# Kernel tuning notes

Measured on AMD Instinct MI355X. Metric: run time of the kernel, lower is better.

## Reference

```python
import jax, jax.numpy as jnp
import numpy as np

D_MODEL = 1024
D_STATE = 16
D_CONV = 4
D_INNER = 2 * D_MODEL          # expand * d_model
DT_RANK = (D_MODEL + 15) // 16 # ceil(d_model/16) = 64
BATCH, SEQLEN = 2, 1024


def setup_inputs() -> dict:
    key = jax.random.key(0)
    ks = jax.random.split(key, 8)
    s = lambda k, shape, scale=0.02: (jax.random.normal(k, shape, jnp.float32) * scale)
    return {
        "hidden_states": jax.random.normal(ks[0], (BATCH, SEQLEN, D_MODEL), jnp.float32),
        "in_proj_w": s(ks[1], (2 * D_INNER, D_MODEL)),
        "conv_w": s(ks[2], (D_INNER, 1, D_CONV), 0.3),   # depthwise conv kernel (O, I/groups=1, K)
        "conv_b": jnp.zeros((D_INNER,), jnp.float32),
        "x_proj_w": s(ks[3], (DT_RANK + 2 * D_STATE, D_INNER)),
        "dt_proj_w": s(ks[4], (D_INNER, DT_RANK), 0.1),
        # inverse-softplus of small dt values, like the torch init
        "dt_proj_b": jax.random.uniform(ks[5], (D_INNER,), jnp.float32, minval=-5.0, maxval=-2.0),
        "A_log": jnp.log(jnp.broadcast_to(jnp.arange(1, D_STATE + 1, dtype=jnp.float32), (D_INNER, D_STATE))),
        "D": jnp.ones((D_INNER,), jnp.float32),
        "out_proj_w": s(ks[6], (D_MODEL, D_INNER)),
    }


def _forward(hidden_states, in_proj_w, conv_w, conv_b, x_proj_w,
             dt_proj_w, dt_proj_b, A_log, D, out_proj_w):
    B, L, _ = hidden_states.shape
    # in_proj -> split into x, z
    xz = hidden_states @ in_proj_w.T                      # [B, L, 2*d_inner]
    x, z = jnp.split(xz, 2, axis=-1)
    # causal depthwise conv1d (pad left d_conv-1, then take first L) + SiLU
    xc = jnp.transpose(x, (0, 2, 1))                      # [B, d_inner, L]
    xc = jax.lax.conv_general_dilated(
        xc, conv_w, window_strides=(1,), padding=[(D_CONV - 1, 0)],
        feature_group_count=D_INNER,
        dimension_numbers=("NCH", "OIH", "NCH")) + conv_b[None, :, None]
    xc = jax.nn.silu(xc)
    u = jnp.transpose(xc, (0, 2, 1)).astype(jnp.float32)  # [B, L, d_inner]
    # x_proj -> dt_low, B, C
    x_dbl = u @ x_proj_w.T                                # [B, L, dt_rank + 2*d_state]
    dt_low, Bp, Cp = jnp.split(x_dbl, [DT_RANK, DT_RANK + D_STATE], axis=-1)
    dt = dt_low @ dt_proj_w.T + dt_proj_b                 # [B, L, d_inner]
    # NOTE: original adds dt_proj.bias AGAIN as delta_bias inside the scan, then softplus
    delta = jax.nn.softplus(dt + dt_proj_b)
    A = -jnp.exp(A_log.astype(jnp.float32))               # [d_inner, d_state]
    # discretization
    dA = jnp.exp(jnp.einsum("bld,dn->lbdn", delta, A))    # [L, B, d, n]
    dBu = jnp.einsum("bld,bln,bld->lbdn", delta, Bp.astype(jnp.float32), u)
    C_t = jnp.transpose(Cp.astype(jnp.float32), (1, 0, 2))  # [L, B, n]

    def step(state, inp):
        a, b, c = inp
        state = a * state + b                             # [B, d, n]
        y = jnp.einsum("bdn,bn->bd", state, c)
        return state, y

    x0 = jnp.zeros((B, D_INNER, D_STATE), jnp.float32)
    _, ys = jax.lax.scan(step, x0, (dA, dBu, C_t))        # ys: [L, B, d]
    y = jnp.transpose(ys, (1, 0, 2))                      # [B, L, d]
    y = y + u * D.astype(jnp.float32)                     # skip connection
    y = y * jax.nn.silu(z.astype(jnp.float32))            # gating
    y = y.astype(hidden_states.dtype)
    return y @ out_proj_w.T                               # [B, L, d_model]


def reference(hidden_states, in_proj_w, conv_w, conv_b, x_proj_w,
              dt_proj_w, dt_proj_b, A_log, D, out_proj_w):
    return _forward(hidden_states, in_proj_w, conv_w, conv_b, x_proj_w,
                    dt_proj_w, dt_proj_b, A_log, D, out_proj_w)
```

## Files before the change

### kernel.cpp

```cpp
#include <hip/hip_runtime.h>
#include <hip/hip_bf16.h>
#include <math.h>

#define BATCH   2
#define SEQLEN  1024
#define DMODEL  1024
#define DINNER  2048
#define DSTATE  16
#define DTRANK  64
#define XPAD    128
#define MROWS   (BATCH*SEQLEN)
#define NSEG    8
#define SEGLEN  (SEQLEN/NSEG)
#define XP_SPLIT  16

typedef float    f32x4  __attribute__((ext_vector_type(4)));
typedef _Float16 f16x8  __attribute__((ext_vector_type(8)));
typedef _Float16 f16x4  __attribute__((ext_vector_type(4)));

template<int EPI>
__global__ __launch_bounds__(256) void pgemm(
    const _Float16* __restrict__ A, int lda,
    const _Float16* __restrict__ W, int ldw,
    float* __restrict__ C, int ldc, int K,
    const float* __restrict__ bias, _Float16* __restrict__ C16, size_t zstride)
{
  constexpr int APS = 520;
  constexpr int BPS = 1032;
  __shared__ _Float16 As[2][8 * APS];
  __shared__ _Float16 Bs[2][8 * BPS];

  const int t  = threadIdx.x;
  const int m0 = blockIdx.y * 64, n0 = blockIdx.x * 128;
  const int kchunk = K / gridDim.z;
  const int kbeg = blockIdx.z * kchunk;
  const int nIter = kchunk / 64;

  const int kb = t & 7;
  const int r0 = t >> 3;
  const _Float16* gA = A + (size_t)(m0 + r0) * lda + kbeg + kb * 8;
  const _Float16* gB = W + (size_t)(n0 + r0) * ldw + kbeg + kb * 8;
  const size_t a32 = (size_t)32 * lda;
  const size_t b32 = (size_t)32 * ldw;
  const int aoff = kb * APS + r0 * 8;
  const int boff = kb * BPS + r0 * 8;

  {
    f16x8 a0 = *(const f16x8*)(gA);
    f16x8 a1 = *(const f16x8*)(gA + a32);
    f16x8 b0 = *(const f16x8*)(gB);
    f16x8 b1 = *(const f16x8*)(gB + b32);
    f16x8 b2 = *(const f16x8*)(gB + 2 * b32);
    f16x8 b3 = *(const f16x8*)(gB + 3 * b32);
    gA += 64; gB += 64;
    *(f16x8*)&As[0][aoff]       = a0;
    *(f16x8*)&As[0][aoff + 256] = a1;
    *(f16x8*)&Bs[0][boff]       = b0;
    *(f16x8*)&Bs[0][boff + 256] = b1;
    *(f16x8*)&Bs[0][boff + 512] = b2;
    *(f16x8*)&Bs[0][boff + 768] = b3;
  }

  const int lane = t & 63, wvi = t >> 6;
  const int wn = wvi * 32;
  const int lm = lane & 15, lk = lane >> 4;

  f32x4 acc[4][2] = {};

  for (int it = 0; it < nIter; ++it) {
    __syncthreads();
    const bool more = (it + 1 < nIter);
    f16x8 a0, a1, b0, b1, b2, b3;
    if (more) {
      a0 = *(const f16x8*)(gA);
      a1 = *(const f16x8*)(gA + a32);
      b0 = *(const f16x8*)(gB);
      b1 = *(const f16x8*)(gB + b32);
      b2 = *(const f16x8*)(gB + 2 * b32);
      b3 = *(const f16x8*)(gB + 3 * b32);
      gA += 64; gB += 64;
    }
    const int cb = it & 1;
#pragma unroll
    for (int s = 0; s < 2; ++s) {
      f16x8 av[4], bv[2];
#pragma unroll
      for (int i = 0; i < 4; ++i)
        av[i] = *(const f16x8*)&As[cb][(s * 4 + lk) * APS + (i * 16 + lm) * 8];
#pragma unroll
      for (int j = 0; j < 2; ++j)
        bv[j] = *(const f16x8*)&Bs[cb][(s * 4 + lk) * BPS + (wn + j * 16 + lm) * 8];
#pragma unroll
      for (int i = 0; i < 4; ++i)
#pragma unroll
        for (int j = 0; j < 2; ++j)
          acc[i][j] = __builtin_amdgcn_mfma_f32_16x16x32_f16(av[i], bv[j], acc[i][j], 0, 0, 0);
    }
    if (more) {
      const int nb = (it + 1) & 1;
      *(f16x8*)&As[nb][aoff]       = a0;
      *(f16x8*)&As[nb][aoff + 256] = a1;
      *(f16x8*)&Bs[nb][boff]       = b0;
      *(f16x8*)&Bs[nb][boff + 256] = b1;
      *(f16x8*)&Bs[nb][boff + 512] = b2;
      *(f16x8*)&Bs[nb][boff + 768] = b3;
    }
  }

  float* Cz = C + (size_t)blockIdx.z * zstride;
#pragma unroll
  for (int i = 0; i < 4; ++i) {
    const int mrow = m0 + i * 16 + lk * 4;
#pragma unroll
    for (int j = 0; j < 2; ++j) {
      const int col = n0 + wn + j * 16 + lm;
#pragma unroll
      for (int r = 0; r < 4; ++r) {
        float v = acc[i][j][r];
        size_t off = (size_t)(mrow + r) * ldc + col;
        if constexpr (EPI == 0) {
          Cz[off] = v;
        } else if constexpr (EPI == 2) {
          float x = v + 2.f * bias[col];
          Cz[off] = (x > 20.f) ? x : log1pf(__expf(x));
        } else {
          C16[off] = (_Float16)v;
        }
      }
    }
  }
}

#define R0 (MROWS * DMODEL / 4)
#define R1 (2 * DINNER * DMODEL / 4)
#define R2 (DMODEL * DINNER / 4)
#define R3 (DINNER * DTRANK / 4)
#define R4 (XPAD * DINNER / 4)
#define F2H_TOTAL (R0 + R1 + R2 + R3 + R4)

__global__ __launch_bounds__(256) void f2h_all(
    const float* __restrict__ hid, const float* __restrict__ w_in,
    const float* __restrict__ w_out, const float* __restrict__ w_dt,
    const float* __restrict__ w_xp,
    _Float16* __restrict__ hid16, _Float16* __restrict__ w_in16,
    _Float16* __restrict__ w_out16, _Float16* __restrict__ w_dt16,
    _Float16* __restrict__ w_xp16)
{
  int i = blockIdx.x * 256 + threadIdx.x;
  const float* src; _Float16* dst; int off;
  if (i < R0)                     { src = hid;   dst = hid16;   off = i; }
  else if (i < R0+R1)             { src = w_in;  dst = w_in16;  off = i - R0; }
  else if (i < R0+R1+R2)          { src = w_out; dst = w_out16; off = i - (R0+R1); }
  else if (i < R0+R1+R2+R3)       { src = w_dt;  dst = w_dt16;  off = i - (R0+R1+R2); }
  else if (i < F2H_TOTAL) {
    off = i - (R0+R1+R2+R3);
    int r = (off * 4) >> 11;
    f16x4 h = {0, 0, 0, 0};
    if (r < 96) {
      float4 v = ((const float4*)w_xp)[off];
      h = (f16x4){(_Float16)v.x, (_Float16)v.y, (_Float16)v.z, (_Float16)v.w};
    }
    ((f16x4*)w_xp16)[off] = h;
    return;
  } else return;
  float4 v = ((const float4*)src)[off];
  ((f16x4*)dst)[off] = (f16x4){(_Float16)v.x, (_Float16)v.y, (_Float16)v.z, (_Float16)v.w};
}

__global__ __launch_bounds__(256) void reduce_xdbl(
    const float* __restrict__ part,
    float* __restrict__ xdbl32, _Float16* __restrict__ xdbl16)
{
  int i = blockIdx.x * 256 + threadIdx.x;
  f32x4 s = ((const f32x4*)part)[i];
#pragma unroll
  for (int z = 1; z < XP_SPLIT; ++z)
    s += ((const f32x4*)part)[(size_t)z * (MROWS * XPAD / 4) + i];
  ((f32x4*)xdbl32)[i] = s;
  int col4 = (i & 31) * 4;
  if (col4 < DTRANK) {
    int row = i >> 5;
    *(f16x4*)&xdbl16[(size_t)row * DTRANK + col4] =
        (f16x4){(_Float16)s.x, (_Float16)s.y, (_Float16)s.z, (_Float16)s.w};
  }
}

__global__ __launch_bounds__(256) void conv_silu(
    const _Float16* __restrict__ xz16,
    const float* __restrict__ conv_w,
    const float* __restrict__ conv_b,
    _Float16* __restrict__ u16)
{
  const int idx = blockIdx.x * 256 + threadIdx.x;
  const int d   = idx & (DINNER - 1);
  const int row = idx >> 11;
  const int l   = row & (SEQLEN - 1);
  float s = conv_b[d];
#pragma unroll
  for (int k = 0; k < 4; ++k) {
    int lt = l + k - 3;
    if (lt >= 0)
      s = fmaf((float)xz16[(size_t)(row + k - 3) * (2 * DINNER) + d],
               conv_w[d * 4 + k], s);
  }
  float v = s / (1.f + __expf(-s));
  u16[idx] = (_Float16)v;
}

__device__ __forceinline__ float row_sum16(float x) {
  int v = __builtin_bit_cast(int, x);
  x += __builtin_bit_cast(float, __builtin_amdgcn_update_dpp(0, v, 0x128, 0xF, 0xF, true));
  v = __builtin_bit_cast(int, x);
  x += __builtin_bit_cast(float, __builtin_amdgcn_update_dpp(0, v, 0x124, 0xF, 0xF, true));
  v = __builtin_bit_cast(int, x);
  x += __builtin_bit_cast(float, __builtin_amdgcn_update_dpp(0, v, 0x4E, 0xF, 0xF, true));
  v = __builtin_bit_cast(int, x);
  x += __builtin_bit_cast(float, __builtin_amdgcn_update_dpp(0, v, 0xB1, 0xF, 0xF, true));
  return x;
}

__global__ __launch_bounds__(256) void scan_part1(
    const float* __restrict__ delta,
    const _Float16* __restrict__ u16,
    const float* __restrict__ x_dbl,
    const float* __restrict__ A_log,
    float* __restrict__ pbuf, float* __restrict__ ebuf)
{
  const int t = threadIdx.x;
  const int c = t >> 4, n = t & 15;
  const int bb = blockIdx.x;
  const int seg = bb >> 8;
  const int r = bb & 255;
  const int b = r >> 7;
  const int d_base = (r & 127) * 16;

  const float A_dn = -__expf(A_log[(d_base + c) * DSTATE + n]);
  float s = 0.f, p = 1.f;

  __shared__ __align__(16) float dl[16 * 68];
  __shared__ __align__(16) float ul[16 * 68];
  __shared__ __align__(16) float Bl[16 * 68];

  const int i_st = t >> 2;
  const int cc = (t & 3) * 4;

  for (int l0 = seg * SEGLEN; l0 < seg * SEGLEN + SEGLEN; l0 += 64) {
    const int row = b * SEQLEN + l0 + i_st;
    {
      float4 dv = *(const float4*)&delta[(size_t)row * DINNER + d_base + cc];
      f16x4  uh = *(const f16x4*)&u16[(size_t)row * DINNER + d_base + cc];
      float4 Bv = *(const float4*)&x_dbl[(size_t)row * XPAD + DTRANK + cc];
      dl[(cc+0)*68 + i_st] = dv.x; dl[(cc+1)*68 + i_st] = dv.y;
      dl[(cc+2)*68 + i_st] = dv.z; dl[(cc+3)*68 + i_st] = dv.w;
      ul[(cc+0)*68 + i_st] = (float)uh[0]; ul[(cc+1)*68 + i_st] = (float)uh[1];
      ul[(cc+2)*68 + i_st] = (float)uh[2]; ul[(cc+3)*68 + i_st] = (float)uh[3];
      Bl[(cc+0)*68 + i_st] = Bv.x; Bl[(cc+1)*68 + i_st] = Bv.y;
      Bl[(cc+2)*68 + i_st] = Bv.z; Bl[(cc+3)*68 + i_st] = Bv.w;
    }
    __syncthreads();
#pragma unroll
    for (int i0 = 0; i0 < 64; i0 += 4) {
      f32x4 dv4 = *(const f32x4*)&dl[c * 68 + i0];
      f32x4 uv4 = *(const f32x4*)&ul[c * 68 + i0];
      f32x4 Bv4 = *(const f32x4*)&Bl[n * 68 + i0];
#pragma unroll
      for (int rr = 0; rr < 4; ++rr) {
        float dA = __expf(dv4[rr] * A_dn);
        s = fmaf(dA, s, dv4[rr] * Bv4[rr] * uv4[rr]);
        p *= dA;
      }
    }
    __syncthreads();
  }
  const int peIdx = (r * NSEG + seg) * 256 + t;
  pbuf[peIdx] = p;
  ebuf[peIdx] = s;
}

__global__ __launch_bounds__(256) void scan_part2(
    const float* __restrict__ delta,
    const _Float16* __restrict__ u16,
    const _Float16* __restrict__ xz16,
    const float* __restrict__ x_dbl,
    const float* __restrict__ A_log,
    const float* __restrict__ Dp,
    const float* __restrict__ pbuf,
    const float* __restrict__ ebuf,
    _Float16* __restrict__ y16)
{
  const int t = threadIdx.x;
  const int c = t >> 4, n = t & 15;
  const int bb = blockIdx.x;
  const int seg = bb >> 8;
  const int r = bb & 255;
  const int b = r >> 7;
  const int d_base = (r & 127) * 16;

  const float A_dn = -__expf(A_log[(d_base + c) * DSTATE + n]);

  float s = 0.f;
  {
    const int base = r * NSEG * 256 + t;
    for (int k = 0; k < seg; ++k)
      s = fmaf(pbuf[base + k * 256], s, ebuf[base + k * 256]);
  }

  __shared__ __align__(16) float dl[16 * 68];
  __shared__ __align__(16) float ul[16 * 68];
  __shared__ __align__(16) float Bl[16 * 68];
  __shared__ __align__(16) float Cl[16 * 68];
  __shared__ __align__(16) float yl[16 * 68];
  __shared__ __align__(16) float z_s[64 * 16];
  __shared__ float Dp_s[16];

  if (t < 16) Dp_s[t] = Dp[d_base + t];

  const int i_st = t >> 2;
  const int cc = (t & 3) * 4;

  for (int l0 = seg * SEGLEN; l0 < seg * SEGLEN + SEGLEN; l0 += 64) {
    const int row = b * SEQLEN + l0 + i_st;
    {
      float4 dv = *(const float4*)&delta[(size_t)row * DINNER + d_base + cc];
      f16x4  uh = *(const f16x4*)&u16[(size_t)row * DINNER + d_base + cc];
      float4 Bv = *(const float4*)&x_dbl[(size_t)row * XPAD + DTRANK + cc];
      float4 Cv = *(const float4*)&x_dbl[(size_t)row * XPAD + DTRANK + DSTATE + cc];
      f16x4  zh = *(const f16x4*)&xz16[(size_t)row * (2 * DINNER) + DINNER + d_base + cc];
      dl[(cc+0)*68 + i_st] = dv.x; dl[(cc+1)*68 + i_st] = dv.y;
      dl[(cc+2)*68 + i_st] = dv.z; dl[(cc+3)*68 + i_st] = dv.w;
      ul[(cc+0)*68 + i_st] = (float)uh[0]; ul[(cc+1)*68 + i_st] = (float)uh[1];
      ul[(cc+2)*68 + i_st] = (float)uh[2]; ul[(cc+3)*68 + i_st] = (float)uh[3];
      Bl[(cc+0)*68 + i_st] = Bv.x; Bl[(cc+1)*68 + i_st] = Bv.y;
      Bl[(cc+2)*68 + i_st] = Bv.z; Bl[(cc+3)*68 + i_st] = Bv.w;
      Cl[(cc+0)*68 + i_st] = Cv.x; Cl[(cc+1)*68 + i_st] = Cv.y;
      Cl[(cc+2)*68 + i_st] = Cv.z; Cl[(cc+3)*68 + i_st] = Cv.w;
      float4 zv = make_float4((float)zh[0], (float)zh[1], (float)zh[2], (float)zh[3]);
      *(float4*)&z_s[t * 4] = zv;
    }
    __syncthreads();

#pragma unroll
    for (int i0 = 0; i0 < 64; i0 += 4) {
      f32x4 dv4 = *(const f32x4*)&dl[c * 68 + i0];
      f32x4 uv4 = *(const f32x4*)&ul[c * 68 + i0];
      f32x4 Bv4 = *(const f32x4*)&Bl[n * 68 + i0];
      f32x4 Cv4 = *(const f32x4*)&Cl[n * 68 + i0];
      f32x4 py;
#pragma unroll
      for (int rr = 0; rr < 4; ++rr) {
        float dA = __expf(dv4[rr] * A_dn);
        s = fmaf(dA, s, dv4[rr] * Bv4[rr] * uv4[rr]);
        py[rr] = row_sum16(s * Cv4[rr]);
      }
      if (n == 0) *(f32x4*)&yl[c * 68 + i0] = py;
    }
    __syncthreads();

#pragma unroll
    for (int k = 0; k < 4; ++k) {
      int o = t + 256 * k;
      int i = o >> 4, c2 = o & 15;
      float ssum = yl[c2 * 68 + i];
      float uv = ul[c2 * 68 + i];
      float zv = z_s[o];
      float yv = fmaf(uv, Dp_s[c2], ssum);
      yv *= zv / (1.f + __expf(-zv));
      y16[(size_t)(b * SEQLEN + l0 + i) * DINNER + d_base + c2] = (_Float16)yv;
    }
    __syncthreads();
  }
}

extern "C" void kernel_launch(void* const* d_in, const int* in_sizes, int n_in,
                              void* d_out, int out_size, void* d_ws, size_t ws_size,
                              hipStream_t stream)
{
  const float* hidden     = (const float*)d_in[0];
  const float* in_proj_w  = (const float*)d_in[1];
  const float* conv_w     = (const float*)d_in[2];
  const float* conv_b     = (const float*)d_in[3];
  const float* x_proj_w   = (const float*)d_in[4];
  const float* dt_proj_w  = (const float*)d_in[5];
  const float* dt_proj_b  = (const float*)d_in[6];
  const float* A_log      = (const float*)d_in[7];
  const float* Dp         = (const float*)d_in[8];
  const float* out_proj_w = (const float*)d_in[9];
  float* out = (float*)d_out;

  char* p = (char*)d_ws;
  _Float16* xz16   = (_Float16*)p;  p += (size_t)MROWS * 2 * DINNER * 2;
  _Float16* u16    = (_Float16*)p;  p += (size_t)MROWS * DINNER * 2;
  float*    xdbl32 = (float*)p;     p += (size_t)MROWS * XPAD * 4;
  float*    delta  = (float*)p;     p += (size_t)MROWS * DINNER * 4;
  _Float16* h16    = (_Float16*)p;  p += (size_t)MROWS * DMODEL * 2;
  _Float16* win16  = (_Float16*)p;  p += (size_t)2 * DINNER * DMODEL * 2;
  _Float16* wout16 = (_Float16*)p;  p += (size_t)DMODEL * DINNER * 2;
  _Float16* wdt16  = (_Float16*)p;  p += (size_t)DINNER * DTRANK * 2;
  _Float16* wxp16  = (_Float16*)p;  p += (size_t)XPAD * DINNER * 2;
  _Float16* xdbl16 = (_Float16*)p;  p += (size_t)MROWS * DTRANK * 2;
  _Float16* y16    = (_Float16*)p;  p += (size_t)MROWS * DINNER * 2;
  float*    pbuf   = (float*)p;     p += (size_t)256 * NSEG * 256 * 4;
  float*    ebuf   = (float*)p;     p += (size_t)256 * NSEG * 256 * 4;
  float*    xp_part = delta;

  f2h_all<<<(F2H_TOTAL + 255) / 256, 256, 0, stream>>>(
      hidden, in_proj_w, out_proj_w, dt_proj_w, x_proj_w,
      h16, win16, wout16, wdt16, wxp16);

  pgemm<4><<<dim3(2 * DINNER / 128, MROWS / 64, 1), 256, 0, stream>>>(
      h16, DMODEL, win16, DMODEL, nullptr, 2 * DINNER, DMODEL, nullptr, xz16, 0);

  conv_silu<<<(MROWS * DINNER) / 256, 256, 0, stream>>>(xz16, conv_w, conv_b, u16);

  pgemm<0><<<dim3(1, MROWS / 64, XP_SPLIT), 256, 0, stream>>>(
      u16, DINNER, wxp16, DINNER, xp_part, XPAD, DINNER, nullptr, nullptr,
      (size_t)MROWS * XPAD);

  reduce_xdbl<<<(MROWS * XPAD / 4) / 256, 256, 0, stream>>>(xp_part, xdbl32, xdbl16);

  pgemm<2><<<dim3(DINNER / 128, MROWS / 64, 1), 256, 0, stream>>>(
      xdbl16, DTRANK, wdt16, DTRANK, delta, DINNER, DTRANK, dt_proj_b, nullptr, 0);

  scan_part1<<<256 * NSEG, 256, 0, stream>>>(delta, u16, xdbl32, A_log, pbuf, ebuf);
  scan_part2<<<256 * NSEG, 256, 0, stream>>>(delta, u16, xz16, xdbl32, A_log, Dp,
                                             pbuf, ebuf, y16);

  pgemm<0><<<dim3(DMODEL / 128, MROWS / 64, 1), 256, 0, stream>>>(
      y16, DINNER, wout16, DINNER, out, DMODEL, DINNER, nullptr, nullptr, 0);
}
```

Before: 252.6 us.

## Add 128x128-tile GEMM for in_proj and split-K out_proj with reduction

Adds a 128x128 block-tile MFMA GEMM kernel with four 64x64 warp tiles and uses it for the large in_proj GEMM, so each operand load from global memory feeds more MFMAs. The out_proj GEMM also moves to the larger tile, but with a 2-way K split writing partials into the now-dead xz16 buffer, followed by a separate reduce kernel. The larger tiles cut the grid size, which the out_proj split-K is meant to offset. The cost is an extra launch plus extra fp32 traffic for the partial sums, and higher register and LDS use per block, which lowers occupancy.

Result: no change. 250.7 us (-0.7%).

```diff
diff --git a/kernel.cpp b/kernel.cpp
--- a/kernel.cpp
+++ b/kernel.cpp
@@ -13,13 +13,14 @@
 #define NSEG    8
 #define SEGLEN  (SEQLEN/NSEG)
 #define XP_SPLIT  16
+#define OUT_SPLIT 2
 
 typedef float    f32x4  __attribute__((ext_vector_type(4)));
 typedef _Float16 f16x8  __attribute__((ext_vector_type(8)));
 typedef _Float16 f16x4  __attribute__((ext_vector_type(4)));
 
 template<int EPI>
-__global__ __launch_bounds__(256) void pgemm(
+__global__ __launch_bounds__(256) void pgemm64(
     const _Float16* __restrict__ A, int lda,
     const _Float16* __restrict__ W, int ldw,
     float* __restrict__ C, int ldc, int K,
@@ -120,9 +121,112 @@
         size_t off = (size_t)(mrow + r) * ldc + col;
         if constexpr (EPI == 0) {
           Cz[off] = v;
-        } else if constexpr (EPI == 2) {
+        } else {
           float x = v + 2.f * bias[col];
           Cz[off] = (x > 20.f) ? x : log1pf(__expf(x));
+        }
+      }
+    }
+  }
+}
+
+template<int EPI>
+__global__ __launch_bounds__(256) void pgemm128(
+    const _Float16* __restrict__ A, int lda,
+    const _Float16* __restrict__ W, int ldw,
+    float* __restrict__ C, int ldc, int K,
+    _Float16* __restrict__ C16, size_t zstride)
+{
+  constexpr int PS = 1032;
+  __shared__ _Float16 As[2][8 * PS];
+  __shared__ _Float16 Bs[2][8 * PS];
+
+  const int t  = threadIdx.x;
+  const int m0 = blockIdx.y * 128, n0 = blockIdx.x * 128;
+  const int kchunk = K / gridDim.z;
+  const int kbeg = blockIdx.z * kchunk;
+  const int nIter = kchunk / 64;
+
+  const int kb = t & 7;
+  const int r0 = t >> 3;
+  const _Float16* gA = A + (size_t)(m0 + r0) * lda + kbeg + kb * 8;
+  const _Float16* gB = W + (size_t)(n0 + r0) * ldw + kbeg + kb * 8;
+  const size_t a32 = (size_t)32 * lda;
+  const size_t b32 = (size_t)32 * ldw;
+  const int soff = kb * PS + r0 * 8;
+
+  {
+    f16x8 ar[4], br[4];
+#pragma unroll
+    for (int j = 0; j < 4; ++j) {
+      ar[j] = *(const f16x8*)(gA + j * a32);
+      br[j] = *(const f16x8*)(gB + j * b32);
+    }
+    gA += 64; gB += 64;
+#pragma unroll
+    for (int j = 0; j < 4; ++j) {
+      *(f16x8*)&As[0][soff + j * 256] = ar[j];
+      *(f16x8*)&Bs[0][soff + j * 256] = br[j];
+    }
+  }
+
+  const int lane = t & 63, wvi = t >> 6;
+  const int wm = (wvi >> 1) * 64, wn = (wvi & 1) * 64;
+  const int lm = lane & 15, lk = lane >> 4;
+
+  f32x4 acc[4][4] = {};
+
+  for (int it = 0; it < nIter; ++it) {
+    __syncthreads();
+    const bool more = (it + 1 < nIter);
+    f16x8 ar[4], br[4];
+    if (more) {
+#pragma unroll
+      for (int j = 0; j < 4; ++j) {
+        ar[j] = *(const f16x8*)(gA + j * a32);
+        br[j] = *(const f16x8*)(gB + j * b32);
+      }
+      gA += 64; gB += 64;
+    }
+    const int cb = it & 1;
+#pragma unroll
+    for (int s = 0; s < 2; ++s) {
+      f16x8 av[4], bv[4];
+#pragma unroll
+      for (int i = 0; i < 4; ++i)
+        av[i] = *(const f16x8*)&As[cb][(s * 4 + lk) * PS + (wm + i * 16 + lm) * 8];
+#pragma unroll
+      for (int j = 0; j < 4; ++j)
+        bv[j] = *(const f16x8*)&Bs[cb][(s * 4 + lk) * PS + (wn + j * 16 + lm) * 8];
+#pragma unroll
+      for (int i = 0; i < 4; ++i)
+#pragma unroll
+        for (int j = 0; j < 4; ++j)
+          acc[i][j] = __builtin_amdgcn_mfma_f32_16x16x32_f16(av[i], bv[j], acc[i][j], 0, 0, 0);
+    }
+    if (more) {
+      const int nb = (it + 1) & 1;
+#pragma unroll
+      for (int j = 0; j < 4; ++j) {
+        *(f16x8*)&As[nb][soff + j * 256] = ar[j];
+        *(f16x8*)&Bs[nb][soff + j * 256] = br[j];
+      }
+    }
+  }
+
+  float* Cz = C + (size_t)blockIdx.z * zstride;
+#pragma unroll
+  for (int i = 0; i < 4; ++i) {
+    const int mrow = m0 + wm + i * 16 + lk * 4;
+#pragma unroll
+    for (int j = 0; j < 4; ++j) {
+      const int col = n0 + wn + j * 16 + lm;
+#pragma unroll
+      for (int r = 0; r < 4; ++r) {
+        float v = acc[i][j][r];
+        size_t off = (size_t)(mrow + r) * ldc + col;
+        if constexpr (EPI == 0) {
+          Cz[off] = v;
         } else {
           C16[off] = (_Float16)v;
         }
@@ -183,6 +287,17 @@
     *(f16x4*)&xdbl16[(size_t)row * DTRANK + col4] =
         (f16x4){(_Float16)s.x, (_Float16)s.y, (_Float16)s.z, (_Float16)s.w};
   }
+}
+
+__global__ __launch_bounds__(256) void reduce_out(
+    const float* __restrict__ part, float* __restrict__ out)
+{
+  int i = blockIdx.x * 256 + threadIdx.x;
+  f32x4 s = ((const f32x4*)part)[i];
+#pragma unroll
+  for (int z = 1; z < OUT_SPLIT; ++z)
+    s += ((const f32x4*)part)[(size_t)z * (MROWS * DMODEL / 4) + i];
+  ((f32x4*)out)[i] = s;
 }
 
 __global__ __launch_bounds__(256) void conv_silu(
@@ -401,30 +516,34 @@
   _Float16* y16    = (_Float16*)p;  p += (size_t)MROWS * DINNER * 2;
   float*    pbuf   = (float*)p;     p += (size_t)256 * NSEG * 256 * 4;
   float*    ebuf   = (float*)p;     p += (size_t)256 * NSEG * 256 * 4;
-  float*    xp_part = delta;
+  float*    xp_part  = delta;
+  float*    out_part = (float*)xz16;
 
   f2h_all<<<(F2H_TOTAL + 255) / 256, 256, 0, stream>>>(
       hidden, in_proj_w, out_proj_w, dt_proj_w, x_proj_w,
       h16, win16, wout16, wdt16, wxp16);
 
-  pgemm<4><<<dim3(2 * DINNER / 128, MROWS / 64, 1), 256, 0, stream>>>(
-      h16, DMODEL, win16, DMODEL, nullptr, 2 * DINNER, DMODEL, nullptr, xz16, 0);
+  pgemm128<4><<<dim3(4096 / 128, MROWS / 128, 1), 256, 0, stream>>>(
+      h16, DMODEL, win16, DMODEL, nullptr, 4096, DMODEL, xz16, 0);
 
   conv_silu<<<(MROWS * DINNER) / 256, 256, 0, stream>>>(xz16, conv_w, conv_b, u16);
 
-  pgemm<0><<<dim3(1, MROWS / 64, XP_SPLIT), 256, 0, stream>>>(
+  pgemm64<0><<<dim3(1, MROWS / 64, XP_SPLIT), 256, 0, stream>>>(
       u16, DINNER, wxp16, DINNER, xp_part, XPAD, DINNER, nullptr, nullptr,
       (size_t)MROWS * XPAD);
 
   reduce_xdbl<<<(MROWS * XPAD / 4) / 256, 256, 0, stream>>>(xp_part, xdbl32, xdbl16);
 
-  pgemm<2><<<dim3(DINNER / 128, MROWS / 64, 1), 256, 0, stream>>>(
+  pgemm64<2><<<dim3(DINNER / 128, MROWS / 64, 1), 256, 0, stream>>>(
       xdbl16, DTRANK, wdt16, DTRANK, delta, DINNER, DTRANK, dt_proj_b, nullptr, 0);
 
   scan_part1<<<256 * NSEG, 256, 0, stream>>>(delta, u16, xdbl32, A_log, pbuf, ebuf);
   scan_part2<<<256 * NSEG, 256, 0, stream>>>(delta, u16, xz16, xdbl32, A_log, Dp,
                                              pbuf, ebuf, y16);
 
-  pgemm<0><<<dim3(DMODEL / 128, MROWS / 64, 1), 256, 0, stream>>>(
-      y16, DINNER, wout16, DINNER, out, DMODEL, DINNER, nullptr, nullptr, 0);
-}
+  pgemm128<0><<<dim3(DMODEL / 128, MROWS / 128, OUT_SPLIT), 256, 0, stream>>>(
+      y16, DINNER, wout16, DINNER, out_part, DMODEL, DINNER, nullptr,
+      (size_t)MROWS * DMODEL);
+
+  reduce_out<<<(MROWS * DMODEL / 4) / 256, 256, 0, stream>>>(out_part, out);
+}
```
